# Kernel tuning notes

Measured on AMD Instinct MI355X. Metric: run time of the kernel, lower is better.

The kernel has to match this reference:

```python
import jax, jax.numpy as jnp
import numpy as np

BITWIDTH = 8
Q_FRAC = BITWIDTH - 4                       # fractional bits of output quantizer
Q_SCALE = 2.0 ** Q_FRAC                     # 16
QMAX = (2 ** (BITWIDTH - 1) - 1) / Q_SCALE  # 7.9375 (overflow clamp on accumulator)
QMIN = -8.0                                 # underflow clamp / accumulator init
LUT_IN_SCALE = 4096.0                       # diff quantized to Q12 index
LUT_IN_MAX = 32767.0                        # index clamp
LUT_OUT_SCALE = 65536.0                     # look_up (= table/2) lives on a 1/65536 grid


def _lut(diff):
    # Emulates the hex lookup table: table[i]/2 ~= log(1 + exp(-i/4096)),
    # quantized to the 1/65536 grid (table entries are Q15, then halved).
    d_int = jnp.minimum(jnp.floor(diff * LUT_IN_SCALE), LUT_IN_MAX)
    d_q = d_int / LUT_IN_SCALE
    return jnp.round(jnp.log1p(jnp.exp(-d_q)) * LUT_OUT_SCALE) / LUT_OUT_SCALE


def _quant_feature(x):
    # QuantizeFeature(bitwidth, bitwidth-4): round to 1/16 grid, clamp to int8 range.
    q = jnp.clip(jnp.round(x * Q_SCALE), -(2 ** (BITWIDTH - 1)), 2 ** (BITWIDTH - 1) - 1)
    return q / Q_SCALE


def _quantized_log_softmax(x):
    B, C, H, W = x.shape
    flat = x.reshape(B * C, H, W)  # sequential axis = flattened batch*channel (as in source)
    init = jnp.full((H, W), QMIN, dtype=x.dtype)

    def step(sum_exp, t):  # t: [H, W]
        diff = jnp.abs(sum_exp - t)
        lu = _lut(diff)
        # if sum_exp > t: sum_exp += lu else: sum_exp = t + lu  ==  max(sum_exp, t) + lu
        s = jnp.maximum(sum_exp, t) + lu
        s = jnp.clip(s, QMIN, QMAX)  # overflow/underflow clamps
        return s, None

    sum_exp, _ = jax.lax.scan(step, init, flat)
    # final scalar per spatial location is broadcast to every (b, c)
    return _quant_feature(x - sum_exp[None, None, :, :])


def setup_inputs() -> dict:
    key = jax.random.key(0)
    x = jax.random.normal(key, (4, 64, 384, 384), dtype=jnp.float32)
    return {"x": x}


def reference(x):
    return _quantized_log_softmax(x)
```

## Files before the change

### kernel.cpp

```cpp
#include <hip/hip_runtime.h>
#include <math.h>

#define QLS_T   256
#define QLS_HW  (384 * 384)

#define Q_SCALE      16.0f
#define INV_Q_SCALE  (1.0f / 16.0f)
#define QMAXF        7.9375f
#define QMINF        (-8.0f)
#define LUT_IN_SCALE 4096.0f
#define LUT_IN_MAX   32767.0f
#define INV_LUT_OUT  (1.0f / 65536.0f)

#define NEG_LOG2E_DIV (-1.4426950408889634f / 4096.0f)
#define LN2_X_65536   45426.09375f

__global__ __launch_bounds__(64) void QuantizedLogSoftmax_12970801234623_kernel(
    const float* __restrict__ x, float* __restrict__ out) {
    const int i = blockIdx.x * 64 + threadIdx.x;
    const float* xp = x + i;

    float s = QMINF;
    #pragma unroll 8
    for (int t = 0; t < QLS_T; ++t) {
        float v = xp[t * QLS_HW];
        float diff = fabsf(s - v);
        float d_int = fminf(floorf(diff * LUT_IN_SCALE), LUT_IN_MAX);
        float e  = __builtin_amdgcn_exp2f(d_int * NEG_LOG2E_DIV);
        float lu = rintf(__builtin_amdgcn_logf(1.0f + e) * LN2_X_65536) * INV_LUT_OUT;
        s = fmaxf(s, v) + lu;
        s = fminf(fmaxf(s, QMINF), QMAXF);
    }

    float* op = out + i;
    #pragma unroll 4
    for (int t = 0; t < QLS_T; ++t) {
        float v = xp[t * QLS_HW];
        float q = fminf(fmaxf(rintf((v - s) * Q_SCALE), -128.0f), 127.0f);
        __builtin_nontemporal_store(q * INV_Q_SCALE, op + t * QLS_HW);
    }
}

extern "C" void kernel_launch(void* const* d_in, const int* in_sizes, int n_in,
                              void* d_out, int out_size, void* d_ws, size_t ws_size,
                              hipStream_t stream) {
    const float* x = (const float*)d_in[0];
    float* out = (float*)d_out;
    const int threads = 64;
    const int blocks = QLS_HW / threads;
    QuantizedLogSoftmax_12970801234623_kernel<<<blocks, threads, 0, stream>>>(x, out);
}
```

Before: 270.6 us.

## Split sequential log-sum scan into parallel chunks combined through shared memory

Splits the 256-step serial scan into 8 chunks of 32 steps, one wavefront per chunk inside a 512-thread block. Each chunk's partial sum starts from the QMIN init, and the partials are then merged with the same step function through shared memory. Each thread keeps its 32 inputs in registers, so the second global read of x for the output pass goes away. The quantized, clamped recurrence is not exactly associative, so results may differ slightly from the strictly sequential reference.

```diff
diff --git a/kernel.cpp b/kernel.cpp
--- a/kernel.cpp
+++ b/kernel.cpp
@@ -3,6 +3,8 @@
 
 #define QLS_T   256
 #define QLS_HW  (384 * 384)
+#define CHUNK   8
+#define TPC     (QLS_T / CHUNK)
 
 #define Q_SCALE      16.0f
 #define INV_Q_SCALE  (1.0f / 16.0f)
@@ -15,29 +17,44 @@
 #define NEG_LOG2E_DIV (-1.4426950408889634f / 4096.0f)
 #define LN2_X_65536   45426.09375f
 
-__global__ __launch_bounds__(64) void QuantizedLogSoftmax_12970801234623_kernel(
+__device__ __forceinline__ float qls_step(float s, float v) {
+    float diff = fabsf(s - v);
+    float d_int = fminf(floorf(diff * LUT_IN_SCALE), LUT_IN_MAX);
+    float e  = __builtin_amdgcn_exp2f(d_int * NEG_LOG2E_DIV);
+    float lu = rintf(__builtin_amdgcn_logf(1.0f + e) * LN2_X_65536) * INV_LUT_OUT;
+    s = fmaxf(s, v) + lu;
+    return fminf(fmaxf(s, QMINF), QMAXF);
+}
+
+__global__ __launch_bounds__(512, 4) void qls_chunked_kernel(
     const float* __restrict__ x, float* __restrict__ out) {
-    const int i = blockIdx.x * 64 + threadIdx.x;
-    const float* xp = x + i;
+    const int lane  = threadIdx.x & 63;
+    const int chunk = threadIdx.x >> 6;
+    const int loc   = blockIdx.x * 64 + lane;
+    const size_t base = (size_t)loc + (size_t)chunk * TPC * QLS_HW;
+    const float* xp = x + base;
+
+    float v[TPC];
+    #pragma unroll
+    for (int k = 0; k < TPC; ++k) v[k] = xp[(size_t)k * QLS_HW];
 
     float s = QMINF;
-    #pragma unroll 8
-    for (int t = 0; t < QLS_T; ++t) {
-        float v = xp[t * QLS_HW];
-        float diff = fabsf(s - v);
-        float d_int = fminf(floorf(diff * LUT_IN_SCALE), LUT_IN_MAX);
-        float e  = __builtin_amdgcn_exp2f(d_int * NEG_LOG2E_DIV);
-        float lu = rintf(__builtin_amdgcn_logf(1.0f + e) * LN2_X_65536) * INV_LUT_OUT;
-        s = fmaxf(s, v) + lu;
-        s = fminf(fmaxf(s, QMINF), QMAXF);
-    }
+    #pragma unroll
+    for (int k = 0; k < TPC; ++k) s = qls_step(s, v[k]);
 
-    float* op = out + i;
-    #pragma unroll 4
-    for (int t = 0; t < QLS_T; ++t) {
-        float v = xp[t * QLS_HW];
-        float q = fminf(fmaxf(rintf((v - s) * Q_SCALE), -128.0f), 127.0f);
-        __builtin_nontemporal_store(q * INV_Q_SCALE, op + t * QLS_HW);
+    __shared__ float part[CHUNK][64];
+    part[chunk][lane] = s;
+    __syncthreads();
+
+    float tot = part[0][lane];
+    #pragma unroll
+    for (int c = 1; c < CHUNK; ++c) tot = qls_step(tot, part[c][lane]);
+
+    float* op = out + base;
+    #pragma unroll
+    for (int k = 0; k < TPC; ++k) {
+        float q = fminf(fmaxf(rintf((v[k] - tot) * Q_SCALE), -128.0f), 127.0f);
+        __builtin_nontemporal_store(q * INV_Q_SCALE, op + (size_t)k * QLS_HW);
     }
 }
 
@@ -46,7 +63,6 @@
                               hipStream_t stream) {
     const float* x = (const float*)d_in[0];
     float* out = (float*)d_out;
-    const int threads = 64;
-    const int blocks = QLS_HW / threads;
-    QuantizedLogSoftmax_12970801234623_kernel<<<blocks, threads, 0, stream>>>(x, out);
+    const int blocks = QLS_HW / 64;
+    qls_chunked_kernel<<<blocks, 512, 0, stream>>>(x, out);
 }
```

New measurement: 268.0 us, median of 2. No clear change (-0.9%).
